# Kernel tuning notes

Hardware: AMD Instinct MI355X
Metric: run time of the kernel (lower is better)

## Reference

```python
import jax, jax.numpy as jnp
import numpy as np

BOUND = 100.0
ALPHA = 0.1
SMOOTH = 1e-05


def setup_inputs() -> dict:
    key = jax.random.key(0)
    k1, k2 = jax.random.split(key)
    B, T, H, W = 8, 16, 512, 512
    inp = jax.random.normal(k1, (B, T, H, W), dtype=jnp.float32)
    tgt = jax.random.uniform(k2, (B, T, H, W), dtype=jnp.float32)
    return {"input": inp, "target": tgt}


def _bce_with_logits(x, t):
    # stable: max(x,0) - x*t + log1p(exp(-|x|)), mean over all elements
    return jnp.mean(jnp.maximum(x, 0.0) - x * t + jnp.log1p(jnp.exp(-jnp.abs(x))))


def reference(input, target):
    B = input.shape[0]
    # --- BCEDiceLoss ---
    bce = _bce_with_logits(input, target)
    p = jax.nn.sigmoid(input).reshape(B, -1)
    t = target.reshape(B, -1)
    intersection = jnp.sum(p * t, axis=1)
    dice_per = (2.0 * intersection + SMOOTH) / (jnp.sum(p, axis=1) + jnp.sum(t, axis=1) + SMOOTH)
    dice = 1.0 - jnp.sum(dice_per) / B
    dice_loss = 0.5 * bce + dice
    # --- sequential size loss (on raw logits, as in original) ---
    s = jnp.sum(input, axis=(2, 3))          # [B, T] per-frame sums
    d = jnp.abs(jnp.diff(s, axis=1))          # [B, T-1]
    ssl = jnp.sum(jax.nn.relu(d - BOUND) ** 2)
    return dice_loss + ALPHA * ssl
```

## Files before the change

### kernel.cpp

```cpp
#include <hip/hip_runtime.h>
#include <math.h>

#define B_   8
#define T_   16
#define HW_  262144
#define N_   (B_*T_*HW_)
#define CHUNKS_PER_FRAME 16
#define NBLOCKS (B_*T_*CHUNKS_PER_FRAME)
#define CHUNK_ELEMS (HW_/CHUNKS_PER_FRAME)
#define THREADS 256

#define BOUND_  100.0f
#define ALPHA_  0.1f
#define SMOOTH_ 1e-5f

__device__ __forceinline__ float wave_reduce(float v) {
    #pragma unroll
    for (int off = 32; off >= 1; off >>= 1)
        v += __shfl_down(v, off, 64);
    return v;
}

__global__ void __launch_bounds__(THREADS)
partials_kernel(const float* __restrict__ x, const float* __restrict__ tg,
                float* __restrict__ ws) {
    const int bid = blockIdx.x;
    const int tid = threadIdx.x;
    const size_t base = (size_t)bid * CHUNK_ELEMS;
    const float4* __restrict__ x4 = (const float4*)(x + base);
    const float4* __restrict__ t4 = (const float4*)(tg + base);

    float s_bce = 0.f, s_pt = 0.f, s_p = 0.f, s_t = 0.f, s_x = 0.f;

    const int n4 = CHUNK_ELEMS / 4;
    for (int i = tid; i < n4; i += THREADS) {
        float4 xv = x4[i];
        float4 tv = t4[i];
        float xs[4] = {xv.x, xv.y, xv.z, xv.w};
        float ts[4] = {tv.x, tv.y, tv.z, tv.w};
        #pragma unroll
        for (int j = 0; j < 4; ++j) {
            float xx = xs[j], tt = ts[j];
            float ax = fabsf(xx);
            float e  = __expf(-ax);
            s_bce += fmaxf(xx, 0.f) - xx * tt + __logf(1.f + e);
            float inv = __fdividef(1.f, 1.f + e);
            float sig = (xx >= 0.f) ? inv : e * inv;
            s_pt += sig * tt;
            s_p  += sig;
            s_t  += tt;
            s_x  += xx;
        }
    }

    __shared__ float red[4][5];
    float v[5] = {s_bce, s_pt, s_p, s_t, s_x};
    const int lane = tid & 63, wv = tid >> 6;
    #pragma unroll
    for (int q = 0; q < 5; ++q) {
        float r = wave_reduce(v[q]);
        if (lane == 0) red[wv][q] = r;
    }
    __syncthreads();
    if (tid == 0) {
        #pragma unroll
        for (int q = 0; q < 5; ++q) {
            float s = red[0][q] + red[1][q] + red[2][q] + red[3][q];
            ws[q * NBLOCKS + bid] = s;
        }
    }
}

__global__ void __launch_bounds__(1024)
finalize_kernel(const float* __restrict__ ws, float* __restrict__ out) {
    __shared__ float buf[NBLOCKS];
    __shared__ float red[1024];
    __shared__ float frame_s[B_ * T_];
    __shared__ float batch_q[3][B_];
    __shared__ float ssl_sh;

    const int tid = threadIdx.x;

    for (int i = tid; i < NBLOCKS; i += 1024) buf[i] = ws[4 * NBLOCKS + i];
    __syncthreads();
    if (tid < B_ * T_) {
        float s = 0.f;
        #pragma unroll
        for (int j = 0; j < CHUNKS_PER_FRAME; ++j)
            s += buf[tid * CHUNKS_PER_FRAME + j];
        frame_s[tid] = s;
    }
    __syncthreads();

    float sslp = 0.f;
    if (tid < B_ * (T_ - 1)) {
        int b = tid / (T_ - 1), k = tid % (T_ - 1);
        int f = b * T_ + k;
        float d = fabsf(frame_s[f + 1] - frame_s[f]);
        float r = fmaxf(d - BOUND_, 0.f);
        sslp = r * r;
    }
    red[tid] = sslp;
    __syncthreads();
    for (int s1 = 512; s1 > 0; s1 >>= 1) {
        if (tid < s1) red[tid] += red[tid + s1];
        __syncthreads();
    }
    if (tid == 0) ssl_sh = red[0];
    __syncthreads();

    for (int q = 0; q < 3; ++q) {
        for (int i = tid; i < NBLOCKS; i += 1024) buf[i] = ws[(q + 1) * NBLOCKS + i];
        __syncthreads();
        if (tid < B_) {
            float s = 0.f;
            const int per = NBLOCKS / B_;
            for (int j = 0; j < per; ++j) s += buf[tid * per + j];
            batch_q[q][tid] = s;
        }
        __syncthreads();
    }

    float v = 0.f;
    for (int i = tid; i < NBLOCKS; i += 1024) v += ws[i];
    red[tid] = v;
    __syncthreads();
    for (int s1 = 512; s1 > 0; s1 >>= 1) {
        if (tid < s1) red[tid] += red[tid + s1];
        __syncthreads();
    }

    if (tid == 0) {
        float bce = red[0] / (float)N_;
        float dice_sum = 0.f;
        #pragma unroll
        for (int b = 0; b < B_; ++b) {
            float inter = batch_q[0][b];
            float dper = (2.f * inter + SMOOTH_) /
                         (batch_q[1][b] + batch_q[2][b] + SMOOTH_);
            dice_sum += dper;
        }
        float dice = 1.f - dice_sum / (float)B_;
        out[0] = 0.5f * bce + dice + ALPHA_ * ssl_sh;
    }
}

extern "C" void kernel_launch(void* const* d_in, const int* in_sizes, int n_in,
                              void* d_out, int out_size, void* d_ws, size_t ws_size,
                              hipStream_t stream) {
    const float* x  = (const float*)d_in[0];
    const float* tg = (const float*)d_in[1];
    float* ws = (float*)d_ws;
    float* out = (float*)d_out;

    partials_kernel<<<NBLOCKS, THREADS, 0, stream>>>(x, tg, ws);
    finalize_kernel<<<1, 1024, 0, stream>>>(ws, out);
}
```

Before: 56.91 us.

## Fuse finalize into partials kernel via last-block atomic counter

Merges the two kernels into one: each block writes its partial sums, bumps an atomic counter, and the last block to finish performs the final reduction with wave shuffles instead of a 1024-thread shared-memory tree. The main loop now loads two float4 pairs per iteration to raise memory-level parallelism. This removes the second kernel launch and its serial single-block tail, but adds a memset launch for the counter plus fences and an atomic per block.

```diff
diff --git a/kernel.cpp b/kernel.cpp
--- a/kernel.cpp
+++ b/kernel.cpp
@@ -21,127 +21,141 @@
     return v;
 }
 
+struct Acc { float bce, pt, p, t, x; };
+
+__device__ __forceinline__ void accum4(const float4 xv, const float4 tv, Acc& a) {
+    float xs[4] = {xv.x, xv.y, xv.z, xv.w};
+    float ts[4] = {tv.x, tv.y, tv.z, tv.w};
+    #pragma unroll
+    for (int j = 0; j < 4; ++j) {
+        float xx = xs[j], tt = ts[j];
+        float ax = fabsf(xx);
+        float e  = __expf(-ax);
+        a.bce += fmaxf(xx, 0.f) - xx * tt + __logf(1.f + e);
+        float inv = __fdividef(1.f, 1.f + e);
+        float sig = (xx >= 0.f) ? inv : e * inv;
+        a.pt += sig * tt;
+        a.p  += sig;
+        a.t  += tt;
+        a.x  += xx;
+    }
+}
+
 __global__ void __launch_bounds__(THREADS)
-partials_kernel(const float* __restrict__ x, const float* __restrict__ tg,
-                float* __restrict__ ws) {
+fused_kernel(const float* __restrict__ x, const float* __restrict__ tg,
+             float* __restrict__ ws, int* __restrict__ counter,
+             float* __restrict__ out) {
     const int bid = blockIdx.x;
     const int tid = threadIdx.x;
     const size_t base = (size_t)bid * CHUNK_ELEMS;
     const float4* __restrict__ x4 = (const float4*)(x + base);
     const float4* __restrict__ t4 = (const float4*)(tg + base);
 
-    float s_bce = 0.f, s_pt = 0.f, s_p = 0.f, s_t = 0.f, s_x = 0.f;
-
+    Acc a = {0.f, 0.f, 0.f, 0.f, 0.f};
     const int n4 = CHUNK_ELEMS / 4;
-    for (int i = tid; i < n4; i += THREADS) {
-        float4 xv = x4[i];
-        float4 tv = t4[i];
-        float xs[4] = {xv.x, xv.y, xv.z, xv.w};
-        float ts[4] = {tv.x, tv.y, tv.z, tv.w};
-        #pragma unroll
-        for (int j = 0; j < 4; ++j) {
-            float xx = xs[j], tt = ts[j];
-            float ax = fabsf(xx);
-            float e  = __expf(-ax);
-            s_bce += fmaxf(xx, 0.f) - xx * tt + __logf(1.f + e);
-            float inv = __fdividef(1.f, 1.f + e);
-            float sig = (xx >= 0.f) ? inv : e * inv;
-            s_pt += sig * tt;
-            s_p  += sig;
-            s_t  += tt;
-            s_x  += xx;
-        }
+    for (int i = tid; i < n4; i += 2 * THREADS) {
+        float4 xa = x4[i];
+        float4 ta = t4[i];
+        float4 xb = x4[i + THREADS];
+        float4 tb = t4[i + THREADS];
+        accum4(xa, ta, a);
+        accum4(xb, tb, a);
     }
 
     __shared__ float red[4][5];
-    float v[5] = {s_bce, s_pt, s_p, s_t, s_x};
-    const int lane = tid & 63, wv = tid >> 6;
-    #pragma unroll
-    for (int q = 0; q < 5; ++q) {
-        float r = wave_reduce(v[q]);
-        if (lane == 0) red[wv][q] = r;
+    __shared__ int lastf;
+    {
+        float v[5] = {a.bce, a.pt, a.p, a.t, a.x};
+        const int lane = tid & 63, wv = tid >> 6;
+        #pragma unroll
+        for (int q = 0; q < 5; ++q) {
+            float r = wave_reduce(v[q]);
+            if (lane == 0) red[wv][q] = r;
+        }
     }
     __syncthreads();
     if (tid == 0) {
         #pragma unroll
-        for (int q = 0; q < 5; ++q) {
-            float s = red[0][q] + red[1][q] + red[2][q] + red[3][q];
-            ws[q * NBLOCKS + bid] = s;
-        }
+        for (int q = 0; q < 5; ++q)
+            ws[q * NBLOCKS + bid] = red[0][q] + red[1][q] + red[2][q] + red[3][q];
+        __threadfence();
+        int prev = atomicAdd(counter, 1);
+        lastf = (prev == NBLOCKS - 1) ? 1 : 0;
     }
-}
+    __syncthreads();
+    if (!lastf) return;
 
-__global__ void __launch_bounds__(1024)
-finalize_kernel(const float* __restrict__ ws, float* __restrict__ out) {
-    __shared__ float buf[NBLOCKS];
-    __shared__ float red[1024];
+    __threadfence();
+
     __shared__ float frame_s[B_ * T_];
     __shared__ float batch_q[3][B_];
-    __shared__ float ssl_sh;
+    __shared__ float sred[4];
+    __shared__ float ssl_val;
 
-    const int tid = threadIdx.x;
+    const int lane = tid & 63, wv = tid >> 6;
+    const float* wx  = ws + 4 * NBLOCKS;
 
-    for (int i = tid; i < NBLOCKS; i += 1024) buf[i] = ws[4 * NBLOCKS + i];
-    __syncthreads();
     if (tid < B_ * T_) {
         float s = 0.f;
         #pragma unroll
         for (int j = 0; j < CHUNKS_PER_FRAME; ++j)
-            s += buf[tid * CHUNKS_PER_FRAME + j];
+            s += wx[tid * CHUNKS_PER_FRAME + j];
         frame_s[tid] = s;
     }
     __syncthreads();
 
-    float sslp = 0.f;
-    if (tid < B_ * (T_ - 1)) {
-        int b = tid / (T_ - 1), k = tid % (T_ - 1);
-        int f = b * T_ + k;
-        float d = fabsf(frame_s[f + 1] - frame_s[f]);
-        float r = fmaxf(d - BOUND_, 0.f);
-        sslp = r * r;
+    {
+        float sslp = 0.f;
+        if (tid < B_ * (T_ - 1)) {
+            int b = tid / (T_ - 1), k = tid % (T_ - 1);
+            int f = b * T_ + k;
+            float d = fabsf(frame_s[f + 1] - frame_s[f]);
+            float r = fmaxf(d - BOUND_, 0.f);
+            sslp = r * r;
+        }
+        float r = wave_reduce(sslp);
+        if (lane == 0) sred[wv] = r;
     }
-    red[tid] = sslp;
     __syncthreads();
-    for (int s1 = 512; s1 > 0; s1 >>= 1) {
-        if (tid < s1) red[tid] += red[tid + s1];
-        __syncthreads();
+    if (tid == 0) ssl_val = sred[0] + sred[1] + sred[2] + sred[3];
+
+    if (tid < 192) {
+        int seg = tid >> 3;
+        int q = seg >> 3;
+        int b = seg & 7;
+        const float* wq = ws + (q + 1) * NBLOCKS + b * (NBLOCKS / B_);
+        float s = 0.f;
+        #pragma unroll
+        for (int k = 0; k < 32; ++k)
+            s += wq[(tid & 7) * 32 + k];
+        s += __shfl_down(s, 4, 64);
+        s += __shfl_down(s, 2, 64);
+        s += __shfl_down(s, 1, 64);
+        if ((tid & 7) == 0) batch_q[q][b] = s;
     }
-    if (tid == 0) ssl_sh = red[0];
     __syncthreads();
 
-    for (int q = 0; q < 3; ++q) {
-        for (int i = tid; i < NBLOCKS; i += 1024) buf[i] = ws[(q + 1) * NBLOCKS + i];
-        __syncthreads();
-        if (tid < B_) {
-            float s = 0.f;
-            const int per = NBLOCKS / B_;
-            for (int j = 0; j < per; ++j) s += buf[tid * per + j];
-            batch_q[q][tid] = s;
-        }
-        __syncthreads();
+    {
+        float s = 0.f;
+        #pragma unroll
+        for (int k = 0; k < 8; ++k)
+            s += ws[tid * 8 + k];
+        float r = wave_reduce(s);
+        if (lane == 0) sred[wv] = r;
     }
-
-    float v = 0.f;
-    for (int i = tid; i < NBLOCKS; i += 1024) v += ws[i];
-    red[tid] = v;
     __syncthreads();
-    for (int s1 = 512; s1 > 0; s1 >>= 1) {
-        if (tid < s1) red[tid] += red[tid + s1];
-        __syncthreads();
-    }
 
     if (tid == 0) {
-        float bce = red[0] / (float)N_;
+        float bce = (sred[0] + sred[1] + sred[2] + sred[3]) / (float)N_;
         float dice_sum = 0.f;
         #pragma unroll
         for (int b = 0; b < B_; ++b) {
             float inter = batch_q[0][b];
-            float dper = (2.f * inter + SMOOTH_) /
-                         (batch_q[1][b] + batch_q[2][b] + SMOOTH_);
-            dice_sum += dper;
+            dice_sum += (2.f * inter + SMOOTH_) /
+                        (batch_q[1][b] + batch_q[2][b] + SMOOTH_);
         }
         float dice = 1.f - dice_sum / (float)B_;
-        out[0] = 0.5f * bce + dice + ALPHA_ * ssl_sh;
+        out[0] = 0.5f * bce + dice + ALPHA_ * ssl_val;
     }
 }
 
@@ -151,8 +165,9 @@
     const float* x  = (const float*)d_in[0];
     const float* tg = (const float*)d_in[1];
     float* ws = (float*)d_ws;
+    int* counter = (int*)((char*)d_ws + 5 * NBLOCKS * sizeof(float));
     float* out = (float*)d_out;
 
-    partials_kernel<<<NBLOCKS, THREADS, 0, stream>>>(x, tg, ws);
-    finalize_kernel<<<1, 1024, 0, stream>>>(ws, out);
+    hipMemsetAsync(counter, 0, sizeof(int), stream);
+    fused_kernel<<<NBLOCKS, THREADS, 0, stream>>>(x, tg, ws, counter, out);
 }
```

Result: slower. 114.6 us (+101.4%).

## Accumulate per-frame and per-batch partials with atomics, shrink finalize kernel

Applied to the files above, without the earlier changes.

Each block now atomically adds its five partial sums straight into small per-frame, per-batch and global accumulators instead of writing per-block partials to workspace. The finalize kernel becomes a tiny 128-thread kernel that reads about 150 values, with no multi-pass reductions or large shared-memory buffers. This adds a memset launch and 2048 blocks' worth of atomic contention on a few addresses, and makes float summation order nondeterministic.

```diff
diff --git a/kernel.cpp b/kernel.cpp
--- a/kernel.cpp
+++ b/kernel.cpp
@@ -14,6 +14,13 @@
 #define ALPHA_  0.1f
 #define SMOOTH_ 1e-5f
 
+#define ACC_FRAME 0
+#define ACC_PT    128
+#define ACC_P     136
+#define ACC_T     144
+#define ACC_BCE   152
+#define ACC_N     153
+
 __device__ __forceinline__ float wave_reduce(float v) {
     #pragma unroll
     for (int off = 32; off >= 1; off >>= 1)
@@ -23,7 +30,7 @@
 
 __global__ void __launch_bounds__(THREADS)
 partials_kernel(const float* __restrict__ x, const float* __restrict__ tg,
-                float* __restrict__ ws) {
+                float* __restrict__ acc) {
     const int bid = blockIdx.x;
     const int tid = threadIdx.x;
     const size_t base = (size_t)bid * CHUNK_ELEMS;
@@ -63,85 +70,51 @@
     }
     __syncthreads();
     if (tid == 0) {
-        #pragma unroll
-        for (int q = 0; q < 5; ++q) {
-            float s = red[0][q] + red[1][q] + red[2][q] + red[3][q];
-            ws[q * NBLOCKS + bid] = s;
-        }
+        const int frame = bid >> 4;
+        const int batch = bid >> 8;
+        float sb = red[0][0] + red[1][0] + red[2][0] + red[3][0];
+        float sp = red[0][1] + red[1][1] + red[2][1] + red[3][1];
+        float sg = red[0][2] + red[1][2] + red[2][2] + red[3][2];
+        float st = red[0][3] + red[1][3] + red[2][3] + red[3][3];
+        float sx = red[0][4] + red[1][4] + red[2][4] + red[3][4];
+        atomicAdd(&acc[ACC_BCE], sb);
+        atomicAdd(&acc[ACC_PT + batch], sp);
+        atomicAdd(&acc[ACC_P  + batch], sg);
+        atomicAdd(&acc[ACC_T  + batch], st);
+        atomicAdd(&acc[ACC_FRAME + frame], sx);
     }
 }
 
-__global__ void __launch_bounds__(1024)
-finalize_kernel(const float* __restrict__ ws, float* __restrict__ out) {
-    __shared__ float buf[NBLOCKS];
-    __shared__ float red[1024];
-    __shared__ float frame_s[B_ * T_];
-    __shared__ float batch_q[3][B_];
-    __shared__ float ssl_sh;
-
+__global__ void __launch_bounds__(128)
+finalize_kernel(const float* __restrict__ acc, float* __restrict__ out) {
+    __shared__ float sred[2];
     const int tid = threadIdx.x;
-
-    for (int i = tid; i < NBLOCKS; i += 1024) buf[i] = ws[4 * NBLOCKS + i];
-    __syncthreads();
-    if (tid < B_ * T_) {
-        float s = 0.f;
-        #pragma unroll
-        for (int j = 0; j < CHUNKS_PER_FRAME; ++j)
-            s += buf[tid * CHUNKS_PER_FRAME + j];
-        frame_s[tid] = s;
-    }
-    __syncthreads();
+    const int lane = tid & 63, wv = tid >> 6;
 
     float sslp = 0.f;
     if (tid < B_ * (T_ - 1)) {
         int b = tid / (T_ - 1), k = tid % (T_ - 1);
         int f = b * T_ + k;
-        float d = fabsf(frame_s[f + 1] - frame_s[f]);
+        float d = fabsf(acc[ACC_FRAME + f + 1] - acc[ACC_FRAME + f]);
         float r = fmaxf(d - BOUND_, 0.f);
         sslp = r * r;
     }
-    red[tid] = sslp;
-    __syncthreads();
-    for (int s1 = 512; s1 > 0; s1 >>= 1) {
-        if (tid < s1) red[tid] += red[tid + s1];
-        __syncthreads();
-    }
-    if (tid == 0) ssl_sh = red[0];
+    float r = wave_reduce(sslp);
+    if (lane == 0) sred[wv] = r;
     __syncthreads();
 
-    for (int q = 0; q < 3; ++q) {
-        for (int i = tid; i < NBLOCKS; i += 1024) buf[i] = ws[(q + 1) * NBLOCKS + i];
-        __syncthreads();
-        if (tid < B_) {
-            float s = 0.f;
-            const int per = NBLOCKS / B_;
-            for (int j = 0; j < per; ++j) s += buf[tid * per + j];
-            batch_q[q][tid] = s;
-        }
-        __syncthreads();
-    }
-
-    float v = 0.f;
-    for (int i = tid; i < NBLOCKS; i += 1024) v += ws[i];
-    red[tid] = v;
-    __syncthreads();
-    for (int s1 = 512; s1 > 0; s1 >>= 1) {
-        if (tid < s1) red[tid] += red[tid + s1];
-        __syncthreads();
-    }
-
     if (tid == 0) {
-        float bce = red[0] / (float)N_;
+        float ssl = sred[0] + sred[1];
+        float bce = acc[ACC_BCE] / (float)N_;
         float dice_sum = 0.f;
         #pragma unroll
         for (int b = 0; b < B_; ++b) {
-            float inter = batch_q[0][b];
-            float dper = (2.f * inter + SMOOTH_) /
-                         (batch_q[1][b] + batch_q[2][b] + SMOOTH_);
-            dice_sum += dper;
+            float inter = acc[ACC_PT + b];
+            dice_sum += (2.f * inter + SMOOTH_) /
+                        (acc[ACC_P + b] + acc[ACC_T + b] + SMOOTH_);
         }
         float dice = 1.f - dice_sum / (float)B_;
-        out[0] = 0.5f * bce + dice + ALPHA_ * ssl_sh;
+        out[0] = 0.5f * bce + dice + ALPHA_ * ssl;
     }
 }
 
@@ -150,9 +123,10 @@
                               hipStream_t stream) {
     const float* x  = (const float*)d_in[0];
     const float* tg = (const float*)d_in[1];
-    float* ws = (float*)d_ws;
+    float* acc = (float*)d_ws;
     float* out = (float*)d_out;
 
-    partials_kernel<<<NBLOCKS, THREADS, 0, stream>>>(x, tg, ws);
-    finalize_kernel<<<1, 1024, 0, stream>>>(ws, out);
+    hipMemsetAsync(acc, 0, ACC_N * sizeof(float), stream);
+    partials_kernel<<<NBLOCKS, THREADS, 0, stream>>>(x, tg, acc);
+    finalize_kernel<<<1, 128, 0, stream>>>(acc, out);
 }
```

Result: slower. 89.31 us (+56.9%).
